# Performance work log

Measured on AMD Instinct MI355X. Metric: run time of the kernel, lower is better.

## Reference

```python
import jax, jax.numpy as jnp
import numpy as np

HIDDEN = 2048
HEADS = 16
HEAD_DIM = HIDDEN // HEADS  # 128
ROPE_BASE = 10000.0


def _rope_cos_sin(seq_len, head_dim, dtype):
    inv_freq = 1.0 / (ROPE_BASE ** (jnp.arange(0, head_dim, 2, dtype=jnp.float32) / head_dim))
    pos = jnp.arange(seq_len, dtype=jnp.float32)
    freqs = pos[:, None] * inv_freq[None, :]            # [S, D/2]
    emb = jnp.concatenate([freqs, freqs], axis=-1)      # [S, D]
    return jnp.cos(emb).astype(dtype), jnp.sin(emb).astype(dtype)


def _rotate_half(x):
    x1, x2 = jnp.split(x, 2, axis=-1)
    return jnp.concatenate([-x2, x1], axis=-1)


def apply_rope(q, k, seq_len):
    # q, k: [B, H, S, Dh]
    cos, sin = _rope_cos_sin(seq_len, q.shape[-1], q.dtype)
    q = q * cos + _rotate_half(q) * sin
    k = k * cos + _rotate_half(k) * sin
    return q, k


def setup_inputs() -> dict:
    key = jax.random.key(0)
    ks = jax.random.split(key, 5)
    B, S = 2, 2048
    scale = 1.0 / np.sqrt(HIDDEN)
    return {
        "hidden_states": jax.random.normal(ks[0], (B, S, HIDDEN), dtype=jnp.float32),
        "w_qkv": jax.random.normal(ks[1], (3 * HIDDEN, HIDDEN), dtype=jnp.float32) * scale,
        "b_qkv": jnp.zeros((3 * HIDDEN,), dtype=jnp.float32),
        "w_dense": jax.random.normal(ks[2], (HIDDEN, HIDDEN), dtype=jnp.float32) * scale,
        "b_dense": jnp.zeros((HIDDEN,), dtype=jnp.float32),
    }


def reference(hidden_states, w_qkv, b_qkv, w_dense, b_dense):
    B, S, _ = hidden_states.shape
    qkv = hidden_states @ w_qkv.T + b_qkv                      # [B, S, 3*H*Dh]
    qkv = qkv.reshape(B, S, 3, HEADS, HEAD_DIM)
    qkv = jnp.transpose(qkv, (2, 0, 3, 1, 4))                  # [3, B, H, S, Dh]
    q, k, v = qkv[0], qkv[1], qkv[2]

    # pos_encoding.apply_to_qk -> RoPE
    q, k = apply_rope(q, k, S)

    scale = HEAD_DIM ** (-0.5)
    scores = jnp.einsum("bhqd,bhkd->bhqk", q, k) * scale       # [B, H, S, S]

    # pos_encoding.apply_to_scores -> causal additive mask
    causal = jnp.tril(jnp.ones((S, S), dtype=bool))
    scores = jnp.where(causal, scores, jnp.finfo(scores.dtype).min)

    attn = jax.nn.softmax(scores, axis=-1)
    out = jnp.einsum("bhqk,bhkd->bhqd", attn, v)               # [B, H, S, Dh]
    out = jnp.transpose(out, (0, 2, 1, 3)).reshape(B, S, HIDDEN)
    return out @ w_dense.T + b_dense
```

## Files before the change

kernel.cpp:

```cpp
#include <hip/hip_runtime.h>
#include <hip/hip_bf16.h>
#include <stdint.h>

#define HID 2048
#define NHEAD 16
#define DHEAD 128
#define BB 2
#define SS 2048
#define MM (BB*SS)
#define NQKV (3*HID)
#define NT (SS/64)

typedef __attribute__((ext_vector_type(8))) short bf16x8;
typedef __attribute__((ext_vector_type(4))) float f32x4;
typedef unsigned short ushort_t;

__device__ __forceinline__ f32x4 mfma16(bf16x8 a, bf16x8 b, f32x4 c) {
    return __builtin_amdgcn_mfma_f32_16x16x32_bf16(a, b, c, 0, 0, 0);
}

__device__ __forceinline__ float bf2f(ushort_t u) {
    unsigned int x = ((unsigned int)u) << 16;
    return __builtin_bit_cast(float, x);
}
__device__ __forceinline__ ushort_t f2bf(float f) {
    unsigned int x = __builtin_bit_cast(unsigned int, f);
    unsigned int r = (x + 0x7FFFu + ((x >> 16) & 1u)) >> 16;
    return (ushort_t)r;
}

__device__ __forceinline__ unsigned int cvtpk(float lo, float hi) {
    unsigned int r;
    asm volatile("v_cvt_pk_bf16_f32 %0, %1, %2" : "=v"(r) : "v"(lo), "v"(hi));
    return r;
}

__device__ __forceinline__ void cvt8(const float* __restrict__ g, ushort_t* l) {
    float4 a = *(const float4*)g;
    float4 b = *(const float4*)(g + 4);
    union { ushort_t u[8]; uint4 v; } t;
    t.u[0] = f2bf(a.x); t.u[1] = f2bf(a.y); t.u[2] = f2bf(a.z); t.u[3] = f2bf(a.w);
    t.u[4] = f2bf(b.x); t.u[5] = f2bf(b.y); t.u[6] = f2bf(b.z); t.u[7] = f2bf(b.w);
    *(uint4*)l = t.v;
}

__device__ __forceinline__ void gload16(const ushort_t* g, ushort_t* l) {
    __builtin_amdgcn_global_load_lds(
        (const __attribute__((address_space(1))) unsigned int*)(const void*)g,
        (__attribute__((address_space(3))) unsigned int*)(void*)l,
        16, 0, 0);
}

#define WAITV0 asm volatile("s_waitcnt vmcnt(0)" ::: "memory")
#define WAITV4 asm volatile("s_waitcnt vmcnt(4)" ::: "memory")
#define WAITV6 asm volatile("s_waitcnt vmcnt(6)" ::: "memory")
#define WAITV8 asm volatile("s_waitcnt vmcnt(8)" ::: "memory")
#define BAR()  __builtin_amdgcn_s_barrier()

__global__ void cvt3_kernel(const float* __restrict__ a, ushort_t* __restrict__ da, int na,
                            const float* __restrict__ b, ushort_t* __restrict__ db, int nb,
                            const float* __restrict__ c, ushort_t* __restrict__ dc, int nc)
{
    int i = blockIdx.x * blockDim.x + threadIdx.x;
    if (i < na) {
        cvt8(a + (size_t)i * 8, da + (size_t)i * 8);
    } else if (i < na + nb) {
        int j = i - na;
        cvt8(b + (size_t)j * 8, db + (size_t)j * 8);
    } else if (i < na + nb + nc) {
        int j = i - na - nb;
        cvt8(c + (size_t)j * 8, dc + (size_t)j * 8);
    }
}

#define BM 256
#define BN 128
#define BKK 64
#define NTK (HID/BKK)
#define ASZ (BM*BKK)
#define BSZ (BN*BKK)
#define BUFSZ (ASZ+BSZ)

__global__ __launch_bounds__(512, 1) void qkv_gemm_fast(
    const ushort_t* __restrict__ X,
    const ushort_t* __restrict__ W,
    const float* __restrict__ bias,
    ushort_t* __restrict__ qws,
    ushort_t* __restrict__ kws,
    ushort_t* __restrict__ vtws)
{
    __shared__ __align__(16) ushort_t smem[3 * BUFSZ];

    const int tid  = threadIdx.x;
    const int lane = tid & 63;
    const int w    = tid >> 6;
    const int wm   = w >> 1, wn = w & 1;
    const int quad = lane >> 4;
    const int l15  = lane & 15;
    const int sub  = (lane & 7) ^ (lane >> 3);
    const int rloc = lane >> 3;
    const int m0 = blockIdx.y * BM;
    const int n0 = blockIdx.x * BN;
    const bool vmode = (n0 >= 2 * HID);

    const ushort_t* gA = X + (size_t)m0 * HID;
    const ushort_t* gB = W + (size_t)n0 * HID;

    f32x4 acc[4][4];
#pragma unroll
    for (int i = 0; i < 4; i++)
#pragma unroll
        for (int j = 0; j < 4; j++)
#pragma unroll
            for (int e = 0; e < 4; e++) acc[i][j][e] = 0.f;

    auto STAGE = [&](int bufi, int t) {
        ushort_t* lA = smem + bufi * BUFSZ;
        ushort_t* lB = lA + ASZ;
        const ushort_t* ga = gA + t * BKK;
        const ushort_t* gb = gB + t * BKK;
#pragma unroll
        for (int i = 0; i < 4; i++) {
            int blk = w * 4 + i;
            gload16(ga + (size_t)(blk * 8 + rloc) * HID + sub * 8, lA + blk * 512);
        }
#pragma unroll
        for (int i = 0; i < 2; i++) {
            int blk = w * 2 + i;
            gload16(gb + (size_t)(blk * 8 + rloc) * HID + sub * 8, lB + blk * 512);
        }
    };

    auto COMPUTE = [&](int bufi) {
        const ushort_t* lA = smem + bufi * BUFSZ;
        const ushort_t* lB = lA + ASZ;
        bf16x8 af[2][4], bfr[2][4];
#pragma unroll
        for (int kk = 0; kk < 2; kk++) {
            const int cs = ((kk * 4 + quad) ^ (l15 & 7)) << 3;
#pragma unroll
            for (int mb = 0; mb < 4; mb++)
                af[kk][mb] = *(const bf16x8*)(lA + (wm * 64 + mb * 16 + l15) * 64 + cs);
#pragma unroll
            for (int nb = 0; nb < 4; nb++)
                bfr[kk][nb] = *(const bf16x8*)(lB + (wn * 64 + nb * 16 + l15) * 64 + cs);
        }
        __builtin_amdgcn_s_setprio(1);
        if (!vmode) {
#pragma unroll
            for (int kk = 0; kk < 2; kk++)
#pragma unroll
                for (int mb = 0; mb < 4; mb++)
#pragma unroll
                    for (int nb = 0; nb < 4; nb++)
                        acc[mb][nb] = mfma16(af[kk][mb], bfr[kk][nb], acc[mb][nb]);
        } else {
#pragma unroll
            for (int kk = 0; kk < 2; kk++)
#pragma unroll
                for (int mb = 0; mb < 4; mb++)
#pragma unroll
                    for (int nb = 0; nb < 4; nb++)
                        acc[mb][nb] = mfma16(bfr[kk][nb], af[kk][mb], acc[mb][nb]);
        }
        __builtin_amdgcn_s_setprio(0);
    };

    STAGE(0, 0);
    STAGE(1, 1);
    WAITV6;
    BAR();

    int buf = 0;
    for (int t = 0; t < NTK - 2; t++) {
        int b2 = buf + 2; if (b2 >= 3) b2 -= 3;
        STAGE(b2, t + 2);
        COMPUTE(buf);
        WAITV6;
        BAR();
        buf++; if (buf == 3) buf = 0;
    }
    COMPUTE(buf);
    WAITV0;
    BAR();
    buf++; if (buf == 3) buf = 0;
    COMPUTE(buf);

    if (!vmode) {
#pragma unroll
        for (int nb = 0; nb < 4; nb++) {
            int n = n0 + wn * 64 + nb * 16 + l15;
            float bv = bias[n];
            int mat = n >> 11;
            int h   = (n >> 7) & 15;
            int d   = n & 127;
            ushort_t* dst = (mat == 0) ? qws : kws;
#pragma unroll
            for (int mb = 0; mb < 4; mb++) {
#pragma unroll
                for (int r = 0; r < 4; r++) {
                    int m = m0 + wm * 64 + mb * 16 + quad * 4 + r;
                    int b = m >> 11;
                    int s = m & 2047;
                    dst[(((size_t)(b * 16 + h) * SS) + s) * DHEAD + d] =
                        f2bf(acc[mb][nb][r] + bv);
                }
            }
        }
    } else {
        const int b = m0 >> 11;
#pragma unroll
        for (int nb = 0; nb < 4; nb++) {
#pragma unroll
            for (int r = 0; r < 4; r++) {
                int n = n0 + wn * 64 + nb * 16 + quad * 4 + r;
                float bv = bias[n];
                int h = (n >> 7) & 15;
                int d = n & 127;
#pragma unroll
                for (int mb = 0; mb < 4; mb++) {
                    int s = (m0 & 2047) + wm * 64 + mb * 16 + l15;
                    vtws[(((size_t)(b * 16 + h) * DHEAD) + d) * SS + s] =
                        f2bf(acc[mb][nb][r] + bv);
                }
            }
        }
    }
}

__global__ __launch_bounds__(512, 1) void dense_gemm_fast(
    const ushort_t* __restrict__ A,
    const ushort_t* __restrict__ W,
    const float* __restrict__ bias,
    float* __restrict__ out)
{
    __shared__ __align__(16) ushort_t smem[3 * BUFSZ];

    const int tid  = threadIdx.x;
    const int lane = tid & 63;
    const int w    = tid >> 6;
    const int wm   = w >> 1;
    const int wn   = w & 1;
    const int quad = lane >> 4;
    const int l15  = lane & 15;
    const int sub  = (lane & 7) ^ (lane >> 3);
    const int rloc = lane >> 3;
    const int m0 = blockIdx.y * BM;
    const int n0 = blockIdx.x * BN;

    const ushort_t* gA = A + (size_t)m0 * HID;
    const ushort_t* gB = W + (size_t)n0 * HID;

    f32x4 acc[4][4];
#pragma unroll
    for (int i = 0; i < 4; i++)
#pragma unroll
        for (int j = 0; j < 4; j++)
#pragma unroll
            for (int e = 0; e < 4; e++) acc[i][j][e] = 0.f;

    auto STAGE = [&](int bufi, int t) {
        ushort_t* lA = smem + bufi * BUFSZ;
        ushort_t* lB = lA + ASZ;
        const ushort_t* ga = gA + t * BKK;
        const ushort_t* gb = gB + t * BKK;
#pragma unroll
        for (int i = 0; i < 4; i++) {
            int blk = w * 4 + i;
            gload16(ga + (size_t)(blk * 8 + rloc) * HID + sub * 8, lA + blk * 512);
        }
#pragma unroll
        for (int i = 0; i < 2; i++) {
            int blk = w * 2 + i;
            gload16(gb + (size_t)(blk * 8 + rloc) * HID + sub * 8, lB + blk * 512);
        }
    };

    auto COMPUTE = [&](int bufi) {
        const ushort_t* lA = smem + bufi * BUFSZ;
        const ushort_t* lB = lA + ASZ;
        bf16x8 af[2][4], bfr[2][4];
#pragma unroll
        for (int kk = 0; kk < 2; kk++) {
            const int cs = ((kk * 4 + quad) ^ (l15 & 7)) << 3;
#pragma unroll
            for (int mb = 0; mb < 4; mb++)
                af[kk][mb] = *(const bf16x8*)(lA + (wm * 64 + mb * 16 + l15) * 64 + cs);
#pragma unroll
            for (int nb = 0; nb < 4; nb++)
                bfr[kk][nb] = *(const bf16x8*)(lB + (wn * 64 + nb * 16 + l15) * 64 + cs);
        }
        __builtin_amdgcn_s_setprio(1);
#pragma unroll
        for (int kk = 0; kk < 2; kk++)
#pragma unroll
            for (int mb = 0; mb < 4; mb++)
#pragma unroll
                for (int nb = 0; nb < 4; nb++)
                    acc[mb][nb] = mfma16(af[kk][mb], bfr[kk][nb], acc[mb][nb]);
        __builtin_amdgcn_s_setprio(0);
    };

    STAGE(0, 0);
    STAGE(1, 1);
    WAITV6;
    BAR();

    int buf = 0;
    for (int t = 0; t < NTK - 2; t++) {
        int b2 = buf + 2; if (b2 >= 3) b2 -= 3;
        STAGE(b2, t + 2);
        COMPUTE(buf);
        WAITV6;
        BAR();
        buf++; if (buf == 3) buf = 0;
    }
    COMPUTE(buf);
    WAITV0;
    BAR();
    buf++; if (buf == 3) buf = 0;
    COMPUTE(buf);

#pragma unroll
    for (int nb = 0; nb < 4; nb++) {
        int n = n0 + wn * 64 + nb * 16 + l15;
        float bv = bias[n];
#pragma unroll
        for (int mb = 0; mb < 4; mb++) {
#pragma unroll
            for (int r = 0; r < 4; r++) {
                int m = m0 + wm * 64 + mb * 16 + quad * 4 + r;
                out[(size_t)m * HID + n] = acc[mb][nb][r] + bv;
            }
        }
    }
}

__global__ void rope_kernel3(ushort_t* __restrict__ qws, ushort_t* __restrict__ kws)
{
    int t = blockIdx.x * blockDim.x + threadIdx.x;
    int d2g = t & 7;
    int s   = (t >> 3) & 2047;
    int bh0 = (t >> 14) * 4;

    float sn[8], cs[8];
#pragma unroll
    for (int jj = 0; jj < 8; jj++) {
        int d2 = d2g * 8 + jj;
        float inv_freq = exp2f(-(float)d2 * (13.287712379549449f / 64.f));
        float fr = (float)s * inv_freq;
        sincosf(fr, &sn[jj], &cs[jj]);
    }

    size_t base0 = (size_t)s * DHEAD + d2g * 8;
#pragma unroll
    for (int q = 0; q < 4; q++) {
        size_t base = base0 + (size_t)(bh0 + q) * (SS * DHEAD);
        {
            union { ushort_t u[8]; uint4 v; } x1, x2, y1, y2;
            x1.v = *(const uint4*)(qws + base);
            x2.v = *(const uint4*)(qws + base + 64);
#pragma unroll
            for (int jj = 0; jj < 8; jj++) {
                float a = bf2f(x1.u[jj]), b = bf2f(x2.u[jj]);
                y1.u[jj] = f2bf(a * cs[jj] - b * sn[jj]);
                y2.u[jj] = f2bf(b * cs[jj] + a * sn[jj]);
            }
            *(uint4*)(qws + base) = y1.v;
            *(uint4*)(qws + base + 64) = y2.v;
        }
        {
            union { ushort_t u[8]; uint4 v; } x1, x2, y1, y2;
            x1.v = *(const uint4*)(kws + base);
            x2.v = *(const uint4*)(kws + base + 64);
#pragma unroll
            for (int jj = 0; jj < 8; jj++) {
                float a = bf2f(x1.u[jj]), b = bf2f(x2.u[jj]);
                y1.u[jj] = f2bf(a * cs[jj] - b * sn[jj]);
                y2.u[jj] = f2bf(b * cs[jj] + a * sn[jj]);
            }
            *(uint4*)(kws + base) = y1.v;
            *(uint4*)(kws + base + 64) = y2.v;
        }
    }
}

#define LDP 72

__global__ __launch_bounds__(256, 2) void attn_kernel7(
    const ushort_t* __restrict__ qws,
    const ushort_t* __restrict__ kws,
    const ushort_t* __restrict__ vtws,
    ushort_t* __restrict__ aout)
{
    __shared__ __align__(16) ushort_t k_s[2][64 * 128];
    __shared__ __align__(16) ushort_t vt_s[128 * 64];
    __shared__ __align__(16) ushort_t pA_s[4][16 * LDP];
    __shared__ __align__(16) ushort_t pB_s[4][16 * LDP];

    const int tid  = threadIdx.x;
    const int lane = tid & 63;
    const int w    = tid >> 6;
    const int quad = lane >> 4;
    const int l15  = lane & 15;

    const int g  = blockIdx.x;
    const int bh = (g & 7) | (((g >> 3) & 3) << 3);
    const int tA = g >> 5;
    const int tB = NT - 1 - tA;
    const int qA = tA * 64, qB = tB * 64;
    const size_t qk_base = (size_t)bh * SS * DHEAD;

    bf16x8 qa[4], qb[4];
    {
        const ushort_t* rowA = qws + qk_base + (size_t)(qA + w * 16 + l15) * DHEAD;
        const ushort_t* rowB = qws + qk_base + (size_t)(qB + w * 16 + l15) * DHEAD;
#pragma unroll
        for (int kc = 0; kc < 4; kc++) {
            qa[kc] = *(const bf16x8*)(rowA + kc * 32 + quad * 8);
            qb[kc] = *(const bf16x8*)(rowB + kc * 32 + quad * 8);
        }
    }

    bf16x8 ones;
#pragma unroll
    for (int i = 0; i < 8; i++) ones[i] = (short)0x3F80;

    f32x4 oA[8], oB[8], lA, lB;
#pragma unroll
    for (int i = 0; i < 8; i++)
#pragma unroll
        for (int e = 0; e < 4; e++) { oA[i][e] = 0.f; oB[i][e] = 0.f; }
#pragma unroll
    for (int e = 0; e < 4; e++) { lA[e] = 0.f; lB[e] = 0.f; }

    const int srowK = lane >> 4;
    const int srowV = lane >> 3;
    const int ccgV  = (lane & 7) ^ (lane >> 3);

    const int qrA = qA + w * 16 + l15;
    const int qrB = qB + w * 16 + l15;
    const int xorv = l15 & 7;

    const float scale2 = 0.12753102015727466f;
    const float FM = 16.0f;

    auto KSTAGE = [&](int j, int slot) {
        const int kb = j * 64;
#pragma unroll
        for (int i = 0; i < 4; i++) {
            int P = i * 4 + w;
            int row = P * 4 + srowK;
            int ccg = l15 ^ (((P & 1) * 4) + srowK);
            gload16(kws + qk_base + (size_t)(kb + row) * DHEAD + ccg * 8,
                    k_s[slot] + P * 512);
        }
    };
    auto VSTAGE = [&](int j) {
        const int kb = j * 64;
#pragma unroll
        for (int i = 0; i < 4; i++) {
            int P = i * 4 + w;
            int row = P * 8 + srowV;
            gload16(vtws + qk_base + (size_t)row * SS + kb + ccgV * 8,
                    vt_s + P * 512);
        }
    };

    KSTAGE(0, 0);

    for (int j = 0; j <= tB; j++) {
        const int kb = j * 64;
        const int slot = j & 1;

        VSTAGE(j);
        if (j < tB) {
            KSTAGE(j + 1, slot ^ 1);
            WAITV8;
        } else {
            WAITV4;
        }
        BAR();

        f32x4 sA[4], sB[4];
#pragma unroll
        for (int nb = 0; nb < 4; nb++)
#pragma unroll
            for (int e = 0; e < 4; e++) { sA[nb][e] = 0.f; sB[nb][e] = 0.f; }

        const ushort_t* ks = k_s[slot];

        if (j <= tA) {
#pragma unroll
            for (int kc = 0; kc < 4; kc++) {
#pragma unroll
                for (int nb = 0; nb < 4; nb++) {
                    int cc_s = (kc * 4 + quad) ^ xorv;
                    bf16x8 kf = *(const bf16x8*)(ks + (nb * 16 + l15) * 128 + cc_s * 8);
                    sA[nb] = mfma16(kf, qa[kc], sA[nb]);
                    sB[nb] = mfma16(kf, qb[kc], sB[nb]);
                }
            }
#pragma unroll
            for (int nb = 0; nb < 4; nb++) {
                int k0 = kb + nb * 16 + quad * 4;
                float pa[4], pb[4];
#pragma unroll
                for (int r = 0; r < 4; r++) {
                    float ea = exp2f(sA[nb][r] * scale2 - FM);
                    float eb = exp2f(sB[nb][r] * scale2 - FM);
                    pa[r] = (k0 + r <= qrA) ? ea : 0.f;
                    pb[r] = (k0 + r <= qrB) ? eb : 0.f;
                }
                uint2 ua, ub;
                ua.x = cvtpk(pa[0], pa[1]); ua.y = cvtpk(pa[2], pa[3]);
                ub.x = cvtpk(pb[0], pb[1]); ub.y = cvtpk(pb[2], pb[3]);
                *(uint2*)(pA_s[w] + l15 * LDP + nb * 16 + quad * 4) = ua;
                *(uint2*)(pB_s[w] + l15 * LDP + nb * 16 + quad * 4) = ub;
            }
            if (j < tB) { WAITV4; } else { WAITV0; }
            BAR();
#pragma unroll
            for (int kc = 0; kc < 2; kc++) {
                bf16x8 pa = *(const bf16x8*)(pA_s[w] + l15 * LDP + kc * 32 + quad * 8);
                bf16x8 pb = *(const bf16x8*)(pB_s[w] + l15 * LDP + kc * 32 + quad * 8);
                lA = mfma16(pa, ones, lA);
                lB = mfma16(pb, ones, lB);
#pragma unroll
                for (int db = 0; db < 8; db++) {
                    int cc_s = (kc * 4 + quad) ^ xorv;
                    bf16x8 vf = *(const bf16x8*)(vt_s + (db * 16 + l15) * 64 + cc_s * 8);
                    oA[db] = mfma16(pa, vf, oA[db]);
                    oB[db] = mfma16(pb, vf, oB[db]);
                }
            }
        } else {
#pragma unroll
            for (int kc = 0; kc < 4; kc++) {
#pragma unroll
                for (int nb = 0; nb < 4; nb++) {
                    int cc_s = (kc * 4 + quad) ^ xorv;
                    bf16x8 kf = *(const bf16x8*)(ks + (nb * 16 + l15) * 128 + cc_s * 8);
                    sB[nb] = mfma16(kf, qb[kc], sB[nb]);
                }
            }
#pragma unroll
            for (int nb = 0; nb < 4; nb++) {
                int k0 = kb + nb * 16 + quad * 4;
                float pb[4];
#pragma unroll
                for (int r = 0; r < 4; r++) {
                    float eb = exp2f(sB[nb][r] * scale2 - FM);
                    pb[r] = (k0 + r <= qrB) ? eb : 0.f;
                }
                uint2 ub;
                ub.x = cvtpk(pb[0], pb[1]); ub.y = cvtpk(pb[2], pb[3]);
                *(uint2*)(pB_s[w] + l15 * LDP + nb * 16 + quad * 4) = ub;
            }
            if (j < tB) { WAITV4; } else { WAITV0; }
            BAR();
#pragma unroll
            for (int kc = 0; kc < 2; kc++) {
                bf16x8 pb = *(const bf16x8*)(pB_s[w] + l15 * LDP + kc * 32 + quad * 8);
                lB = mfma16(pb, ones, lB);
#pragma unroll
                for (int db = 0; db < 8; db++) {
                    int cc_s = (kc * 4 + quad) ^ xorv;
                    bf16x8 vf = *(const bf16x8*)(vt_s + (db * 16 + l15) * 64 + cc_s * 8);
                    oB[db] = mfma16(pb, vf, oB[db]);
                }
            }
        }
        BAR();
    }

    const int b = bh >> 4;
    const int h = bh & 15;
    float invA[4], invB[4];
#pragma unroll
    for (int r = 0; r < 4; r++) { invA[r] = 1.f / lA[r]; invB[r] = 1.f / lB[r]; }
#pragma unroll
    for (int db = 0; db < 8; db++) {
#pragma unroll
        for (int r = 0; r < 4; r++) {
            int sA_row = qA + w * 16 + quad * 4 + r;
            int sB_row = qB + w * 16 + quad * 4 + r;
            size_t offA = ((size_t)(b * SS + sA_row)) * HID + h * DHEAD + db * 16 + l15;
            size_t offB = ((size_t)(b * SS + sB_row)) * HID + h * DHEAD + db * 16 + l15;
            aout[offA] = f2bf(oA[db][r] * invA[r]);
            aout[offB] = f2bf(oB[db][r] * invB[r]);
        }
    }
}

extern "C" void kernel_launch(void* const* d_in, const int* in_sizes, int n_in,
                              void* d_out, int out_size, void* d_ws, size_t ws_size,
                              hipStream_t stream)
{
    const float* X    = (const float*)d_in[0];
    const float* Wqkv = (const float*)d_in[1];
    const float* bqkv = (const float*)d_in[2];
    const float* Wd   = (const float*)d_in[3];
    const float* bd   = (const float*)d_in[4];
    float* out = (float*)d_out;

    char* ws = (char*)d_ws;
    const size_t MB = 1048576;
    ushort_t* qws  = (ushort_t*)(ws);
    ushort_t* kws  = (ushort_t*)(ws + 16 * MB);
    ushort_t* vtws = (ushort_t*)(ws + 32 * MB);
    ushort_t* aout = (ushort_t*)(ws + 48 * MB);
    ushort_t* Xbf  = (ushort_t*)(ws + 48 * MB);
    ushort_t* Wqbf = (ushort_t*)(ws + 64 * MB);
    ushort_t* Wdbf = (ushort_t*)(ws + 88 * MB);

    const int nX = MM * HID / 8, nWq = NQKV * HID / 8, nWd = HID * HID / 8;
    cvt3_kernel<<<(nX + nWq + nWd + 255) / 256, 256, 0, stream>>>(
        X, Xbf, nX, Wqkv, Wqbf, nWq, Wd, Wdbf, nWd);

    qkv_gemm_fast<<<dim3(NQKV / BN, MM / BM), 512, 0, stream>>>(Xbf, Wqbf, bqkv, qws, kws, vtws);
    rope_kernel3<<<(SS * 8 * 8) / 256, 256, 0, stream>>>(qws, kws);
    attn_kernel7<<<dim3(NT / 2 * BB * NHEAD), 256, 0, stream>>>(qws, kws, vtws, aout);
    dense_gemm_fast<<<dim3(HID / BN, MM / BM), 512, 0, stream>>>(aout, Wdbf, bd, out);
}
```

Baseline: 372.1 us.

## Software-pipeline attention: overlap PV of tile j with QK softmax of tile j+1

Restructures the attention loop into a software pipeline. Each iteration computes P·V for the current key tile and then QK^T plus exp for the next tile. V is now double-buffered, K loads are issued two tiles ahead, and there is one barrier per iteration instead of two. The P staging buffers drop their padded stride in favour of an XOR swizzle to avoid bank conflicts. LDS use grows by an extra 16KB V buffer, which may limit occupancy at two blocks per CU, and the loop now waits on all outstanding loads (vmcnt(0)) every iteration.

```diff
diff --git a/kernel.cpp b/kernel.cpp
--- a/kernel.cpp
+++ b/kernel.cpp
@@ -54,7 +54,6 @@
 #define WAITV0 asm volatile("s_waitcnt vmcnt(0)" ::: "memory")
 #define WAITV4 asm volatile("s_waitcnt vmcnt(4)" ::: "memory")
 #define WAITV6 asm volatile("s_waitcnt vmcnt(6)" ::: "memory")
-#define WAITV8 asm volatile("s_waitcnt vmcnt(8)" ::: "memory")
 #define BAR()  __builtin_amdgcn_s_barrier()
 
 __global__ void cvt3_kernel(const float* __restrict__ a, ushort_t* __restrict__ da, int na,
@@ -385,18 +384,16 @@
     }
 }
 
-#define LDP 72
-
-__global__ __launch_bounds__(256, 2) void attn_kernel7(
+__global__ __launch_bounds__(256, 2) void attn_kernel8(
     const ushort_t* __restrict__ qws,
     const ushort_t* __restrict__ kws,
     const ushort_t* __restrict__ vtws,
     ushort_t* __restrict__ aout)
 {
     __shared__ __align__(16) ushort_t k_s[2][64 * 128];
-    __shared__ __align__(16) ushort_t vt_s[128 * 64];
-    __shared__ __align__(16) ushort_t pA_s[4][16 * LDP];
-    __shared__ __align__(16) ushort_t pB_s[4][16 * LDP];
+    __shared__ __align__(16) ushort_t vt_s[2][128 * 64];
+    __shared__ __align__(16) ushort_t pA_s[4][16 * 64];
+    __shared__ __align__(16) ushort_t pB_s[4][16 * 64];
 
     const int tid  = threadIdx.x;
     const int lane = tid & 63;
@@ -441,6 +438,7 @@
     const int qrA = qA + w * 16 + l15;
     const int qrB = qB + w * 16 + l15;
     const int xorv = l15 & 7;
+    const int pxor = l15 & 7;
 
     const float scale2 = 0.12753102015727466f;
     const float FM = 16.0f;
@@ -456,41 +454,27 @@
                     k_s[slot] + P * 512);
         }
     };
-    auto VSTAGE = [&](int j) {
+    auto VSTAGE = [&](int j, int slot) {
         const int kb = j * 64;
 #pragma unroll
         for (int i = 0; i < 4; i++) {
             int P = i * 4 + w;
             int row = P * 8 + srowV;
             gload16(vtws + qk_base + (size_t)row * SS + kb + ccgV * 8,
-                    vt_s + P * 512);
-        }
-    };
-
-    KSTAGE(0, 0);
-
-    for (int j = 0; j <= tB; j++) {
-        const int kb = j * 64;
-        const int slot = j & 1;
-
-        VSTAGE(j);
-        if (j < tB) {
-            KSTAGE(j + 1, slot ^ 1);
-            WAITV8;
-        } else {
-            WAITV4;
-        }
-        BAR();
-
+                    vt_s[slot] + P * 512);
+        }
+    };
+
+    auto QKSM = [&](int jj) {
+        const int kb = jj * 64;
+        const ushort_t* ks = k_s[jj & 1];
         f32x4 sA[4], sB[4];
 #pragma unroll
         for (int nb = 0; nb < 4; nb++)
 #pragma unroll
             for (int e = 0; e < 4; e++) { sA[nb][e] = 0.f; sB[nb][e] = 0.f; }
 
-        const ushort_t* ks = k_s[slot];
-
-        if (j <= tA) {
+        if (jj <= tA) {
 #pragma unroll
             for (int kc = 0; kc < 4; kc++) {
 #pragma unroll
@@ -515,24 +499,9 @@
                 uint2 ua, ub;
                 ua.x = cvtpk(pa[0], pa[1]); ua.y = cvtpk(pa[2], pa[3]);
                 ub.x = cvtpk(pb[0], pb[1]); ub.y = cvtpk(pb[2], pb[3]);
-                *(uint2*)(pA_s[w] + l15 * LDP + nb * 16 + quad * 4) = ua;
-                *(uint2*)(pB_s[w] + l15 * LDP + nb * 16 + quad * 4) = ub;
-            }
-            if (j < tB) { WAITV4; } else { WAITV0; }
-            BAR();
-#pragma unroll
-            for (int kc = 0; kc < 2; kc++) {
-                bf16x8 pa = *(const bf16x8*)(pA_s[w] + l15 * LDP + kc * 32 + quad * 8);
-                bf16x8 pb = *(const bf16x8*)(pB_s[w] + l15 * LDP + kc * 32 + quad * 8);
-                lA = mfma16(pa, ones, lA);
-                lB = mfma16(pb, ones, lB);
-#pragma unroll
-                for (int db = 0; db < 8; db++) {
-                    int cc_s = (kc * 4 + quad) ^ xorv;
-                    bf16x8 vf = *(const bf16x8*)(vt_s + (db * 16 + l15) * 64 + cc_s * 8);
-                    oA[db] = mfma16(pa, vf, oA[db]);
-                    oB[db] = mfma16(pb, vf, oB[db]);
-                }
+                int hs = ((nb * 2 + (quad >> 1)) ^ pxor) * 8 + (quad & 1) * 4;
+                *(uint2*)(pA_s[w] + l15 * 64 + hs) = ua;
+                *(uint2*)(pB_s[w] + l15 * 64 + hs) = ub;
             }
         } else {
 #pragma unroll
@@ -555,22 +524,56 @@
                 }
                 uint2 ub;
                 ub.x = cvtpk(pb[0], pb[1]); ub.y = cvtpk(pb[2], pb[3]);
-                *(uint2*)(pB_s[w] + l15 * LDP + nb * 16 + quad * 4) = ub;
-            }
-            if (j < tB) { WAITV4; } else { WAITV0; }
-            BAR();
-#pragma unroll
-            for (int kc = 0; kc < 2; kc++) {
-                bf16x8 pb = *(const bf16x8*)(pB_s[w] + l15 * LDP + kc * 32 + quad * 8);
-                lB = mfma16(pb, ones, lB);
+                int hs = ((nb * 2 + (quad >> 1)) ^ pxor) * 8 + (quad & 1) * 4;
+                *(uint2*)(pB_s[w] + l15 * 64 + hs) = ub;
+            }
+        }
+    };
+
+    auto PV = [&](int jj) {
+        const ushort_t* vs = vt_s[jj & 1];
+        const bool dual = (jj <= tA);
+#pragma unroll
+        for (int kc = 0; kc < 2; kc++) {
+            int hp = ((kc * 4 + quad) ^ pxor) * 8;
+            bf16x8 pb = *(const bf16x8*)(pB_s[w] + l15 * 64 + hp);
+            lB = mfma16(pb, ones, lB);
+            if (dual) {
+                bf16x8 pa = *(const bf16x8*)(pA_s[w] + l15 * 64 + hp);
+                lA = mfma16(pa, ones, lA);
 #pragma unroll
                 for (int db = 0; db < 8; db++) {
                     int cc_s = (kc * 4 + quad) ^ xorv;
-                    bf16x8 vf = *(const bf16x8*)(vt_s + (db * 16 + l15) * 64 + cc_s * 8);
+                    bf16x8 vf = *(const bf16x8*)(vs + (db * 16 + l15) * 64 + cc_s * 8);
+                    oA[db] = mfma16(pa, vf, oA[db]);
                     oB[db] = mfma16(pb, vf, oB[db]);
                 }
-            }
-        }
+            } else {
+#pragma unroll
+                for (int db = 0; db < 8; db++) {
+                    int cc_s = (kc * 4 + quad) ^ xorv;
+                    bf16x8 vf = *(const bf16x8*)(vs + (db * 16 + l15) * 64 + cc_s * 8);
+                    oB[db] = mfma16(pb, vf, oB[db]);
+                }
+            }
+        }
+    };
+
+    KSTAGE(0, 0);
+    VSTAGE(0, 0);
+    KSTAGE(1, 1);
+    WAITV4;
+    BAR();
+    QKSM(0);
+    WAITV0;
+    BAR();
+
+    for (int j = 0; j <= tB; j++) {
+        if (j + 1 <= tB) VSTAGE(j + 1, (j + 1) & 1);
+        if (j + 2 <= tB) KSTAGE(j + 2, j & 1);
+        PV(j);
+        if (j + 1 <= tB) QKSM(j + 1);
+        WAITV0;
         BAR();
     }
 
@@ -620,6 +623,6 @@
 
     qkv_gemm_fast<<<dim3(NQKV / BN, MM / BM), 512, 0, stream>>>(Xbf, Wqbf, bqkv, qws, kws, vtws);
     rope_kernel3<<<(SS * 8 * 8) / 256, 256, 0, stream>>>(qws, kws);
-    attn_kernel7<<<dim3(NT / 2 * BB * NHEAD), 256, 0, stream>>>(qws, kws, vtws, aout);
+    attn_kernel8<<<dim3(NT / 2 * BB * NHEAD), 256, 0, stream>>>(qws, kws, vtws, aout);
     dense_gemm_fast<<<dim3(HID / BN, MM / BM), 512, 0, stream>>>(aout, Wdbf, bd, out);
 }
```

After: 361.6 us. 1.03x faster.
